# Kernel optimization log

Hardware: AMD Instinct MI355X
Metric: run time of the kernel (lower is better)

## Reference

```python
import jax, jax.numpy as jnp
import numpy as np

SCALING = 128.0 / 64  # alpha / rank = 2.0
EPS = 1e-8


def setup_inputs() -> dict:
    key = jax.random.key(0)
    ks = jax.random.split(key, 5)
    B, S, D_IN, D_OUT, R = 2, 4096, 4096, 4096, 64
    x = jax.random.normal(ks[0], (B, S, D_IN), dtype=jnp.float32)
    base_output = jax.random.normal(ks[1], (B, S, D_OUT), dtype=jnp.float32)
    base_weight = jax.random.normal(ks[2], (D_OUT, D_IN), dtype=jnp.float32) * 0.02
    lora_A = jax.random.normal(ks[3], (R, D_IN), dtype=jnp.float32) * 0.02
    lora_B = jax.random.normal(ks[4], (D_OUT, R), dtype=jnp.float32) * 0.02
    magnitude = jnp.ones((D_OUT,), dtype=jnp.float32)
    return {"x": x, "base_output": base_output, "base_weight": base_weight,
            "lora_A": lora_A, "lora_B": lora_B, "magnitude": magnitude}


def reference(x, base_output, base_weight, lora_A, lora_B, magnitude):
    # LoRA path: x @ A^T @ B^T, scaled  (dropout p=0 -> identity)
    xa = jnp.einsum('bsd,rd->bsr', x, lora_A)          # [B,S,r]
    delta_v = jnp.einsum('bsr,or->bso', xa, lora_B) * SCALING  # [B,S,out]
    # Updated weight and its per-row L2 norm
    updated_weight = base_weight + (lora_B @ lora_A) * SCALING  # [out,in]
    updated_norm = jnp.sqrt(jnp.sum(updated_weight * updated_weight, axis=1))  # [out]
    mag_scale = magnitude / (updated_norm + EPS)  # [out]
    combined = base_output + delta_v
    return combined * mag_scale[None, None, :]
```

## Files before the change

### kernel.cpp

```cpp
#include <hip/hip_runtime.h>
#include <math.h>

typedef __bf16 bf16x8 __attribute__((ext_vector_type(8)));
typedef float f32x4 __attribute__((ext_vector_type(4)));

#define MFMA16(a, b, c) __builtin_amdgcn_mfma_f32_16x16x32_bf16(a, b, c, 0, 0, 0)

static constexpr int M_TOT = 8192;
static constexpr int DIN = 4096;
static constexpr int DOUT = 4096;
static constexpr int RNK = 64;

__device__ inline unsigned short f2bf(float f) {
    union { float f; unsigned u; } v; v.f = f;
    unsigned r = v.u + 0x7FFFu + ((v.u >> 16) & 1u);
    return (unsigned short)(r >> 16);
}

__global__ __launch_bounds__(256) void k_prep(const float* __restrict__ A,
                                              const float* __restrict__ B,
                                              unsigned short* __restrict__ Afrag,
                                              unsigned short* __restrict__ Atfrag,
                                              unsigned short* __restrict__ Bfrag) {
    int i = blockIdx.x * 256 + threadIdx.x;
    unsigned short ab = f2bf(A[i]);
    int n = i >> 12, k = i & 4095;
    Afrag[(((k >> 5) << 2) + (n >> 4)) * 512 +
          ((((k >> 3) & 3) << 4) + (n & 15)) * 8 + (k & 7)] = ab;
    Atfrag[(((k >> 4) << 1) + (n >> 5)) * 512 +
           ((((n >> 3) & 3) << 4) + (k & 15)) * 8 + (n & 7)] = ab;
    unsigned short bb = f2bf(B[i]);
    int o = i >> 6, r = i & 63;
    Bfrag[(((o >> 4) << 1) + (r >> 5)) * 512 +
          ((((r >> 3) & 3) << 4) + (o & 15)) * 8 + (r & 7)] = bb;
}

__global__ __launch_bounds__(512, 6) void kA(const float* __restrict__ x,
                                             const unsigned short* __restrict__ Afrag,
                                             unsigned short* __restrict__ xafrag,
                                             const float* __restrict__ bw,
                                             const unsigned short* __restrict__ Bfrag,
                                             const unsigned short* __restrict__ Atfrag,
                                             const float* __restrict__ mag,
                                             float* __restrict__ mscale) {
    __shared__ __align__(16) char smem[33792];
    int tid = threadIdx.x;
    int wid = tid >> 6, lane = tid & 63;
    int row = lane & 15, kq = lane >> 4;
    int sr = tid >> 5, sc = (tid & 31) * 4;
    int lane8 = lane * 8;

    if (blockIdx.x < 512) {
        unsigned short (*stage)[520] = (unsigned short (*)[520])smem;
        float (*red)[1024] = (float (*)[1024])smem;
        int m0 = blockIdx.x * 16;
        const float* xrow = x + (size_t)(m0 + sr) * DIN + sc;

        f32x4 acc0 = {0.f, 0.f, 0.f, 0.f};
        f32x4 acc1 = acc0, acc2 = acc0, acc3 = acc0;

        f32x4 r0 = *(const f32x4*)(xrow);
        f32x4 r1 = *(const f32x4*)(xrow + 128);
        f32x4 r2 = *(const f32x4*)(xrow + 256);
        f32x4 r3 = *(const f32x4*)(xrow + 384);

        for (int c = 0; c < 8; ++c) {
            __syncthreads();
            ushort4 h;
            h.x = f2bf(r0[0]); h.y = f2bf(r0[1]); h.z = f2bf(r0[2]); h.w = f2bf(r0[3]);
            *(ushort4*)&stage[sr][sc] = h;
            h.x = f2bf(r1[0]); h.y = f2bf(r1[1]); h.z = f2bf(r1[2]); h.w = f2bf(r1[3]);
            *(ushort4*)&stage[sr][128 + sc] = h;
            h.x = f2bf(r2[0]); h.y = f2bf(r2[1]); h.z = f2bf(r2[2]); h.w = f2bf(r2[3]);
            *(ushort4*)&stage[sr][256 + sc] = h;
            h.x = f2bf(r3[0]); h.y = f2bf(r3[1]); h.z = f2bf(r3[2]); h.w = f2bf(r3[3]);
            *(ushort4*)&stage[sr][384 + sc] = h;
            if (c < 7) {
                const float* nx = xrow + (c + 1) * 512;
                r0 = *(const f32x4*)(nx);
                r1 = *(const f32x4*)(nx + 128);
                r2 = *(const f32x4*)(nx + 256);
                r3 = *(const f32x4*)(nx + 384);
            }
            __syncthreads();
            #pragma unroll
            for (int s = 0; s < 2; ++s) {
                int k0 = wid * 64 + s * 32;
                bf16x8 af = *(const bf16x8*)&stage[row][k0 + kq * 8];
                int ks = (c * 512 + k0) >> 5;
                const unsigned short* ap = Afrag + (size_t)(ks << 2) * 512 + lane8;
                acc0 = MFMA16(af, *(const bf16x8*)(ap), acc0);
                acc1 = MFMA16(af, *(const bf16x8*)(ap + 512), acc1);
                acc2 = MFMA16(af, *(const bf16x8*)(ap + 1024), acc2);
                acc3 = MFMA16(af, *(const bf16x8*)(ap + 1536), acc3);
            }
        }
        __syncthreads();

        int mb = kq * 4;
        #pragma unroll
        for (int rg = 0; rg < 4; ++rg) {
            red[wid][(mb + rg) * 64 + row]      = acc0[rg];
            red[wid][(mb + rg) * 64 + 16 + row] = acc1[rg];
            red[wid][(mb + rg) * 64 + 32 + row] = acc2[rg];
            red[wid][(mb + rg) * 64 + 48 + row] = acc3[rg];
        }
        __syncthreads();
        #pragma unroll
        for (int e = tid; e < 1024; e += 512) {
            float s = 0.f;
            #pragma unroll
            for (int w = 0; w < 8; ++w) s += red[w][e];
            int ml = e >> 6, r = e & 63;
            xafrag[((size_t)blockIdx.x * 2 + (r >> 5)) * 512 +
                   ((((r >> 3) & 3) << 4) + ml) * 8 + (r & 7)] = f2bf(s);
        }
    } else {
        float (*stagef)[516] = (float (*)[516])smem;
        float (*part)[16] = (float (*)[16])(smem + 33024);
        int o0 = (blockIdx.x - 512) * 16;
        int ot = o0 >> 4;

        bf16x8 b0 = *(const bf16x8*)(Bfrag + (size_t)(ot * 2) * 512 + lane8);
        bf16x8 b1 = *(const bf16x8*)(Bfrag + (size_t)(ot * 2 + 1) * 512 + lane8);

        f32x4 nacc = {0.f, 0.f, 0.f, 0.f};
        const float* bwrow = bw + (size_t)(o0 + sr) * DIN + sc;

        f32x4 q0 = *(const f32x4*)(bwrow);
        f32x4 q1 = *(const f32x4*)(bwrow + 128);
        f32x4 q2 = *(const f32x4*)(bwrow + 256);
        f32x4 q3 = *(const f32x4*)(bwrow + 384);

        for (int c = 0; c < 8; ++c) {
            __syncthreads();
            *(f32x4*)&stagef[sr][sc]       = q0;
            *(f32x4*)&stagef[sr][128 + sc] = q1;
            *(f32x4*)&stagef[sr][256 + sc] = q2;
            *(f32x4*)&stagef[sr][384 + sc] = q3;
            if (c < 7) {
                const float* nb = bwrow + (c + 1) * 512;
                q0 = *(const f32x4*)(nb);
                q1 = *(const f32x4*)(nb + 128);
                q2 = *(const f32x4*)(nb + 256);
                q3 = *(const f32x4*)(nb + 384);
            }
            __syncthreads();
            #pragma unroll
            for (int g = 0; g < 4; ++g) {
                int iloc = wid * 64 + g * 16;
                int it = (c * 512 + iloc) >> 4;
                const unsigned short* atp = Atfrag + (size_t)(it * 2) * 512 + lane8;
                bf16x8 a0 = *(const bf16x8*)(atp);
                bf16x8 a1 = *(const bf16x8*)(atp + 512);
                f32x4 d = {0.f, 0.f, 0.f, 0.f};
                d = MFMA16(a0, b0, d);
                d = MFMA16(a1, b1, d);
                f32x4 wv = *(const f32x4*)&stagef[row][iloc + kq * 4];
                #pragma unroll
                for (int rg = 0; rg < 4; ++rg) {
                    float w = wv[rg] + 2.0f * d[rg];
                    nacc[rg] += w * w;
                }
            }
        }
        float ns = nacc[0] + nacc[1] + nacc[2] + nacc[3];
        ns += __shfl_xor(ns, 16, 64);
        ns += __shfl_xor(ns, 32, 64);
        if (kq == 0) part[wid][row] = ns;
        __syncthreads();
        if (tid < 16) {
            float n2 = 0.f;
            #pragma unroll
            for (int w = 0; w < 8; ++w) n2 += part[w][tid];
            mscale[o0 + tid] = mag[o0 + tid] / (sqrtf(n2) + 1e-8f);
        }
    }
}

__global__ __launch_bounds__(256) void kB(const float* __restrict__ base,
                                          const unsigned short* __restrict__ xafrag,
                                          const unsigned short* __restrict__ Bfrag,
                                          const float* __restrict__ mscale,
                                          float* __restrict__ out) {
    __shared__ float dls[32][260];
    int tid = threadIdx.x;
    int wid = tid >> 6, lane = tid & 63;
    int row = lane & 15, kq = lane >> 4;
    int m0 = blockIdx.x * 32;
    int n0 = blockIdx.y * 256;
    int col = n0 + lane * 4;
    int lane8 = lane * 8;

    f32x4 bpre[2][4];
    #pragma unroll
    for (int h = 0; h < 2; ++h)
        #pragma unroll
        for (int r = 0; r < 4; ++r)
            bpre[h][r] = __builtin_nontemporal_load(
                (const f32x4*)(base + (size_t)(m0 + h * 16 + wid * 4 + r) * DOUT + col));
    f32x4 msv = *(const f32x4*)(mscale + col);

    bf16x8 xb0[2], xb1[2];
    #pragma unroll
    for (int h = 0; h < 2; ++h) {
        size_t mt = (size_t)(blockIdx.x * 2 + h);
        xb0[h] = *(const bf16x8*)(xafrag + (mt * 2) * 512 + lane8);
        xb1[h] = *(const bf16x8*)(xafrag + (mt * 2 + 1) * 512 + lane8);
    }

    #pragma unroll
    for (int nt = 0; nt < 4; ++nt) {
        size_t ntg = (size_t)((n0 + wid * 64 + nt * 16) >> 4);
        bf16x8 a0 = *(const bf16x8*)(Bfrag + (ntg * 2) * 512 + lane8);
        bf16x8 a1 = *(const bf16x8*)(Bfrag + (ntg * 2 + 1) * 512 + lane8);
        #pragma unroll
        for (int h = 0; h < 2; ++h) {
            f32x4 acc = {0.f, 0.f, 0.f, 0.f};
            acc = MFMA16(a0, xb0[h], acc);
            acc = MFMA16(a1, xb1[h], acc);
            *(f32x4*)&dls[h * 16 + row][wid * 64 + nt * 16 + kq * 4] = acc;
        }
    }
    __syncthreads();

    #pragma unroll
    for (int h = 0; h < 2; ++h)
        #pragma unroll
        for (int r = 0; r < 4; ++r) {
            int m = h * 16 + wid * 4 + r;
            f32x4 d = *(const f32x4*)&dls[m][lane * 4];
            size_t gidx = (size_t)(m0 + m) * DOUT + col;
            f32x4 o;
            #pragma unroll
            for (int j = 0; j < 4; ++j) o[j] = (bpre[h][r][j] + 2.0f * d[j]) * msv[j];
            __builtin_nontemporal_store(o, (f32x4*)(out + gidx));
        }
}

extern "C" void kernel_launch(void* const* d_in, const int* in_sizes, int n_in,
                              void* d_out, int out_size, void* d_ws, size_t ws_size,
                              hipStream_t stream) {
    const float* x    = (const float*)d_in[0];
    const float* base = (const float*)d_in[1];
    const float* bw   = (const float*)d_in[2];
    const float* lA   = (const float*)d_in[3];
    const float* lB   = (const float*)d_in[4];
    const float* mag  = (const float*)d_in[5];
    float* out = (float*)d_out;

    char* ws = (char*)d_ws;
    unsigned short* Afrag  = (unsigned short*)(ws);
    unsigned short* Atfrag = (unsigned short*)(ws + (512u << 10));
    unsigned short* Bfrag  = (unsigned short*)(ws + (1024u << 10));
    unsigned short* xafrag = (unsigned short*)(ws + (1536u << 10));
    float*          msc    = (float*)(ws + (2560u << 10));

    hipLaunchKernelGGL(k_prep, dim3(1024), dim3(256), 0, stream, lA, lB, Afrag, Atfrag, Bfrag);
    hipLaunchKernelGGL(kA, dim3(512 + 256), dim3(512), 0, stream,
                       x, Afrag, xafrag, bw, Bfrag, Atfrag, mag, msc);
    hipLaunchKernelGGL(kB, dim3(M_TOT / 32, DOUT / 256), dim3(256), 0, stream,
                       base, xafrag, Bfrag, msc, out);
}
```

Measured before the change: 112.1 us.

## Split-K the xA and weight-norm passes into separate wider kernels

Replaces the fused kA kernel with two split-K kernels. k1_xa splits the 4096-wide reduction over x into 4 parts, writes fp32 partials, and a small k1_fin kernel sums them into the bf16 fragment layout. k2_norm splits the weight-norm row reduction into 8 parts, and kB now sums those partials and computes the magnitude scale inline. The aim is more blocks with one-shot loads instead of a serial 8-chunk loop, giving more parallelism and latency hiding. The cost is an extra launch, an 8 MB round trip of fp32 partials, and redundant norm finalisation in every kB block.

```diff
diff --git a/kernel.cpp b/kernel.cpp
--- a/kernel.cpp
+++ b/kernel.cpp
@@ -35,153 +35,143 @@
           ((((r >> 3) & 3) << 4) + (o & 15)) * 8 + (r & 7)] = bb;
 }
 
-__global__ __launch_bounds__(512, 6) void kA(const float* __restrict__ x,
-                                             const unsigned short* __restrict__ Afrag,
-                                             unsigned short* __restrict__ xafrag,
-                                             const float* __restrict__ bw,
-                                             const unsigned short* __restrict__ Bfrag,
-                                             const unsigned short* __restrict__ Atfrag,
-                                             const float* __restrict__ mag,
-                                             float* __restrict__ mscale) {
-    __shared__ __align__(16) char smem[33792];
+__global__ __launch_bounds__(256, 4) void k1_xa(const float* __restrict__ x,
+                                                const unsigned short* __restrict__ Afrag,
+                                                float* __restrict__ pxa) {
+    __shared__ __align__(16) char smem[33024];
+    unsigned short (*stage)[1032] = (unsigned short (*)[1032])smem;
+    float (*red)[1024] = (float (*)[1024])smem;
     int tid = threadIdx.x;
     int wid = tid >> 6, lane = tid & 63;
     int row = lane & 15, kq = lane >> 4;
-    int sr = tid >> 5, sc = (tid & 31) * 4;
     int lane8 = lane * 8;
-
-    if (blockIdx.x < 512) {
-        unsigned short (*stage)[520] = (unsigned short (*)[520])smem;
-        float (*red)[1024] = (float (*)[1024])smem;
-        int m0 = blockIdx.x * 16;
-        const float* xrow = x + (size_t)(m0 + sr) * DIN + sc;
-
-        f32x4 acc0 = {0.f, 0.f, 0.f, 0.f};
-        f32x4 acc1 = acc0, acc2 = acc0, acc3 = acc0;
-
-        f32x4 r0 = *(const f32x4*)(xrow);
-        f32x4 r1 = *(const f32x4*)(xrow + 128);
-        f32x4 r2 = *(const f32x4*)(xrow + 256);
-        f32x4 r3 = *(const f32x4*)(xrow + 384);
-
-        for (int c = 0; c < 8; ++c) {
-            __syncthreads();
-            ushort4 h;
-            h.x = f2bf(r0[0]); h.y = f2bf(r0[1]); h.z = f2bf(r0[2]); h.w = f2bf(r0[3]);
-            *(ushort4*)&stage[sr][sc] = h;
-            h.x = f2bf(r1[0]); h.y = f2bf(r1[1]); h.z = f2bf(r1[2]); h.w = f2bf(r1[3]);
-            *(ushort4*)&stage[sr][128 + sc] = h;
-            h.x = f2bf(r2[0]); h.y = f2bf(r2[1]); h.z = f2bf(r2[2]); h.w = f2bf(r2[3]);
-            *(ushort4*)&stage[sr][256 + sc] = h;
-            h.x = f2bf(r3[0]); h.y = f2bf(r3[1]); h.z = f2bf(r3[2]); h.w = f2bf(r3[3]);
-            *(ushort4*)&stage[sr][384 + sc] = h;
-            if (c < 7) {
-                const float* nx = xrow + (c + 1) * 512;
-                r0 = *(const f32x4*)(nx);
-                r1 = *(const f32x4*)(nx + 128);
-                r2 = *(const f32x4*)(nx + 256);
-                r3 = *(const f32x4*)(nx + 384);
-            }
-            __syncthreads();
-            #pragma unroll
-            for (int s = 0; s < 2; ++s) {
-                int k0 = wid * 64 + s * 32;
-                bf16x8 af = *(const bf16x8*)&stage[row][k0 + kq * 8];
-                int ks = (c * 512 + k0) >> 5;
-                const unsigned short* ap = Afrag + (size_t)(ks << 2) * 512 + lane8;
-                acc0 = MFMA16(af, *(const bf16x8*)(ap), acc0);
-                acc1 = MFMA16(af, *(const bf16x8*)(ap + 512), acc1);
-                acc2 = MFMA16(af, *(const bf16x8*)(ap + 1024), acc2);
-                acc3 = MFMA16(af, *(const bf16x8*)(ap + 1536), acc3);
-            }
+    int mt = blockIdx.x & 511, kpart = blockIdx.x >> 9;
+    int m0 = mt * 16;
+    int sr = tid >> 4, sc = (tid & 15) * 4;
+
+    const float* xp = x + (size_t)(m0 + sr) * DIN + kpart * 1024 + sc;
+    f32x4 r[16];
+    #pragma unroll
+    for (int p = 0; p < 16; ++p) r[p] = *(const f32x4*)(xp + p * 64);
+
+    #pragma unroll
+    for (int p = 0; p < 16; ++p) {
+        ushort4 h;
+        h.x = f2bf(r[p][0]); h.y = f2bf(r[p][1]); h.z = f2bf(r[p][2]); h.w = f2bf(r[p][3]);
+        *(ushort4*)&stage[sr][p * 64 + sc] = h;
+    }
+    __syncthreads();
+
+    f32x4 acc0 = {0.f, 0.f, 0.f, 0.f};
+    f32x4 acc1 = acc0, acc2 = acc0, acc3 = acc0;
+    #pragma unroll
+    for (int s = 0; s < 8; ++s) {
+        bf16x8 af = *(const bf16x8*)&stage[row][wid * 256 + s * 32 + kq * 8];
+        int ks = kpart * 32 + wid * 8 + s;
+        const unsigned short* ap = Afrag + (size_t)(ks << 2) * 512 + lane8;
+        acc0 = MFMA16(af, *(const bf16x8*)(ap), acc0);
+        acc1 = MFMA16(af, *(const bf16x8*)(ap + 512), acc1);
+        acc2 = MFMA16(af, *(const bf16x8*)(ap + 1024), acc2);
+        acc3 = MFMA16(af, *(const bf16x8*)(ap + 1536), acc3);
+    }
+    __syncthreads();
+
+    int mb = kq * 4;
+    #pragma unroll
+    for (int rg = 0; rg < 4; ++rg) {
+        red[wid][(mb + rg) * 64 + row]      = acc0[rg];
+        red[wid][(mb + rg) * 64 + 16 + row] = acc1[rg];
+        red[wid][(mb + rg) * 64 + 32 + row] = acc2[rg];
+        red[wid][(mb + rg) * 64 + 48 + row] = acc3[rg];
+    }
+    __syncthreads();
+    #pragma unroll
+    for (int e = tid; e < 1024; e += 256) {
+        float s = red[0][e] + red[1][e] + red[2][e] + red[3][e];
+        pxa[(size_t)kpart * M_TOT * RNK + (size_t)(m0 + (e >> 6)) * RNK + (e & 63)] = s;
+    }
+}
+
+__global__ __launch_bounds__(256) void k1_fin(const float* __restrict__ pxa,
+                                              unsigned short* __restrict__ xafrag) {
+    int tid = threadIdx.x;
+    int mt = blockIdx.x;
+    int e0 = tid * 4;
+    size_t o = (size_t)(mt * 16 + (e0 >> 6)) * RNK + (e0 & 63);
+    f32x4 s0 = *(const f32x4*)(pxa + o);
+    f32x4 s1 = *(const f32x4*)(pxa + (size_t)M_TOT * RNK + o);
+    f32x4 s2 = *(const f32x4*)(pxa + 2 * (size_t)M_TOT * RNK + o);
+    f32x4 s3 = *(const f32x4*)(pxa + 3 * (size_t)M_TOT * RNK + o);
+    int ml = e0 >> 6, r0 = e0 & 63;
+    ushort4 h;
+    h.x = f2bf(s0[0] + s1[0] + s2[0] + s3[0]);
+    h.y = f2bf(s0[1] + s1[1] + s2[1] + s3[1]);
+    h.z = f2bf(s0[2] + s1[2] + s2[2] + s3[2]);
+    h.w = f2bf(s0[3] + s1[3] + s2[3] + s3[3]);
+    *(ushort4*)&xafrag[((size_t)(mt * 2 + (r0 >> 5))) * 512 +
+                       ((((r0 >> 3) & 3) << 4) + ml) * 8 + (r0 & 7)] = h;
+}
+
+__global__ __launch_bounds__(256, 4) void k2_norm(const float* __restrict__ bw,
+                                                  const unsigned short* __restrict__ Bfrag,
+                                                  const unsigned short* __restrict__ Atfrag,
+                                                  float* __restrict__ pn) {
+    __shared__ __align__(16) char smem[33280];
+    float (*stagef)[516] = (float (*)[516])smem;
+    float (*part)[16] = (float (*)[16])(smem + 33024);
+    int tid = threadIdx.x;
+    int wid = tid >> 6, lane = tid & 63;
+    int row = lane & 15, kq = lane >> 4;
+    int lane8 = lane * 8;
+    int ot = blockIdx.x & 255, ipart = blockIdx.x >> 8;
+    int o0 = ot * 16;
+    int sr = tid >> 4, sc = (tid & 15) * 4;
+
+    const float* bwp = bw + (size_t)(o0 + sr) * DIN + ipart * 512 + sc;
+    f32x4 q[8];
+    #pragma unroll
+    for (int p = 0; p < 8; ++p) q[p] = *(const f32x4*)(bwp + p * 64);
+
+    bf16x8 b0 = *(const bf16x8*)(Bfrag + (size_t)(ot * 2) * 512 + lane8);
+    bf16x8 b1 = *(const bf16x8*)(Bfrag + (size_t)(ot * 2 + 1) * 512 + lane8);
+
+    #pragma unroll
+    for (int p = 0; p < 8; ++p) *(f32x4*)&stagef[sr][p * 64 + sc] = q[p];
+    __syncthreads();
+
+    f32x4 nacc = {0.f, 0.f, 0.f, 0.f};
+    #pragma unroll
+    for (int g = 0; g < 8; ++g) {
+        int iloc = wid * 128 + g * 16;
+        int it = (ipart * 512 + iloc) >> 4;
+        const unsigned short* atp = Atfrag + (size_t)(it * 2) * 512 + lane8;
+        bf16x8 a0 = *(const bf16x8*)(atp);
+        bf16x8 a1 = *(const bf16x8*)(atp + 512);
+        f32x4 d = {0.f, 0.f, 0.f, 0.f};
+        d = MFMA16(a0, b0, d);
+        d = MFMA16(a1, b1, d);
+        f32x4 wv = *(const f32x4*)&stagef[row][iloc + kq * 4];
+        #pragma unroll
+        for (int rg = 0; rg < 4; ++rg) {
+            float w = wv[rg] + 2.0f * d[rg];
+            nacc[rg] += w * w;
         }
-        __syncthreads();
-
-        int mb = kq * 4;
-        #pragma unroll
-        for (int rg = 0; rg < 4; ++rg) {
-            red[wid][(mb + rg) * 64 + row]      = acc0[rg];
-            red[wid][(mb + rg) * 64 + 16 + row] = acc1[rg];
-            red[wid][(mb + rg) * 64 + 32 + row] = acc2[rg];
-            red[wid][(mb + rg) * 64 + 48 + row] = acc3[rg];
-        }
-        __syncthreads();
-        #pragma unroll
-        for (int e = tid; e < 1024; e += 512) {
-            float s = 0.f;
-            #pragma unroll
-            for (int w = 0; w < 8; ++w) s += red[w][e];
-            int ml = e >> 6, r = e & 63;
-            xafrag[((size_t)blockIdx.x * 2 + (r >> 5)) * 512 +
-                   ((((r >> 3) & 3) << 4) + ml) * 8 + (r & 7)] = f2bf(s);
-        }
-    } else {
-        float (*stagef)[516] = (float (*)[516])smem;
-        float (*part)[16] = (float (*)[16])(smem + 33024);
-        int o0 = (blockIdx.x - 512) * 16;
-        int ot = o0 >> 4;
-
-        bf16x8 b0 = *(const bf16x8*)(Bfrag + (size_t)(ot * 2) * 512 + lane8);
-        bf16x8 b1 = *(const bf16x8*)(Bfrag + (size_t)(ot * 2 + 1) * 512 + lane8);
-
-        f32x4 nacc = {0.f, 0.f, 0.f, 0.f};
-        const float* bwrow = bw + (size_t)(o0 + sr) * DIN + sc;
-
-        f32x4 q0 = *(const f32x4*)(bwrow);
-        f32x4 q1 = *(const f32x4*)(bwrow + 128);
-        f32x4 q2 = *(const f32x4*)(bwrow + 256);
-        f32x4 q3 = *(const f32x4*)(bwrow + 384);
-
-        for (int c = 0; c < 8; ++c) {
-            __syncthreads();
-            *(f32x4*)&stagef[sr][sc]       = q0;
-            *(f32x4*)&stagef[sr][128 + sc] = q1;
-            *(f32x4*)&stagef[sr][256 + sc] = q2;
-            *(f32x4*)&stagef[sr][384 + sc] = q3;
-            if (c < 7) {
-                const float* nb = bwrow + (c + 1) * 512;
-                q0 = *(const f32x4*)(nb);
-                q1 = *(const f32x4*)(nb + 128);
-                q2 = *(const f32x4*)(nb + 256);
-                q3 = *(const f32x4*)(nb + 384);
-            }
-            __syncthreads();
-            #pragma unroll
-            for (int g = 0; g < 4; ++g) {
-                int iloc = wid * 64 + g * 16;
-                int it = (c * 512 + iloc) >> 4;
-                const unsigned short* atp = Atfrag + (size_t)(it * 2) * 512 + lane8;
-                bf16x8 a0 = *(const bf16x8*)(atp);
-                bf16x8 a1 = *(const bf16x8*)(atp + 512);
-                f32x4 d = {0.f, 0.f, 0.f, 0.f};
-                d = MFMA16(a0, b0, d);
-                d = MFMA16(a1, b1, d);
-                f32x4 wv = *(const f32x4*)&stagef[row][iloc + kq * 4];
-                #pragma unroll
-                for (int rg = 0; rg < 4; ++rg) {
-                    float w = wv[rg] + 2.0f * d[rg];
-                    nacc[rg] += w * w;
-                }
-            }
-        }
-        float ns = nacc[0] + nacc[1] + nacc[2] + nacc[3];
-        ns += __shfl_xor(ns, 16, 64);
-        ns += __shfl_xor(ns, 32, 64);
-        if (kq == 0) part[wid][row] = ns;
-        __syncthreads();
-        if (tid < 16) {
-            float n2 = 0.f;
-            #pragma unroll
-            for (int w = 0; w < 8; ++w) n2 += part[w][tid];
-            mscale[o0 + tid] = mag[o0 + tid] / (sqrtf(n2) + 1e-8f);
-        }
-    }
+    }
+    float ns = nacc[0] + nacc[1] + nacc[2] + nacc[3];
+    ns += __shfl_xor(ns, 16, 64);
+    ns += __shfl_xor(ns, 32, 64);
+    if (kq == 0) part[wid][row] = ns;
+    __syncthreads();
+    if (tid < 16)
+        pn[ipart * DOUT + o0 + tid] =
+            part[0][tid] + part[1][tid] + part[2][tid] + part[3][tid];
 }
 
 __global__ __launch_bounds__(256) void kB(const float* __restrict__ base,
                                           const unsigned short* __restrict__ xafrag,
                                           const unsigned short* __restrict__ Bfrag,
-                                          const float* __restrict__ mscale,
+                                          const float* __restrict__ pn,
+                                          const float* __restrict__ mag,
                                           float* __restrict__ out) {
     __shared__ float dls[32][260];
     int tid = threadIdx.x;
@@ -199,7 +189,10 @@
         for (int r = 0; r < 4; ++r)
             bpre[h][r] = __builtin_nontemporal_load(
                 (const f32x4*)(base + (size_t)(m0 + h * 16 + wid * 4 + r) * DOUT + col));
-    f32x4 msv = *(const f32x4*)(mscale + col);
+    f32x4 pnv[8];
+    #pragma unroll
+    for (int p = 0; p < 8; ++p) pnv[p] = *(const f32x4*)(pn + p * DOUT + col);
+    f32x4 mg = *(const f32x4*)(mag + col);
 
     bf16x8 xb0[2], xb1[2];
     #pragma unroll
@@ -223,6 +216,15 @@
         }
     }
     __syncthreads();
+
+    f32x4 msv;
+    #pragma unroll
+    for (int j = 0; j < 4; ++j) {
+        float n2 = 0.f;
+        #pragma unroll
+        for (int p = 0; p < 8; ++p) n2 += pnv[p][j];
+        msv[j] = mg[j] / (sqrtf(n2) + 1e-8f);
+    }
 
     #pragma unroll
     for (int h = 0; h < 2; ++h)
@@ -254,11 +256,13 @@
     unsigned short* Atfrag = (unsigned short*)(ws + (512u << 10));
     unsigned short* Bfrag  = (unsigned short*)(ws + (1024u << 10));
     unsigned short* xafrag = (unsigned short*)(ws + (1536u << 10));
-    float*          msc    = (float*)(ws + (2560u << 10));
+    float*          pxa    = (float*)(ws + (2560u << 10));
+    float*          pn     = (float*)(ws + (10752u << 10));
 
     hipLaunchKernelGGL(k_prep, dim3(1024), dim3(256), 0, stream, lA, lB, Afrag, Atfrag, Bfrag);
-    hipLaunchKernelGGL(kA, dim3(512 + 256), dim3(512), 0, stream,
-                       x, Afrag, xafrag, bw, Bfrag, Atfrag, mag, msc);
+    hipLaunchKernelGGL(k1_xa, dim3(2048), dim3(256), 0, stream, x, Afrag, pxa);
+    hipLaunchKernelGGL(k2_norm, dim3(2048), dim3(256), 0, stream, bw, Bfrag, Atfrag, pn);
+    hipLaunchKernelGGL(k1_fin, dim3(512), dim3(256), 0, stream, pxa, xafrag);
     hipLaunchKernelGGL(kB, dim3(M_TOT / 32, DOUT / 256), dim3(256), 0, stream,
-                       base, xafrag, Bfrag, msc, out);
-}
+                       base, xafrag, Bfrag, pn, mag, out);
+}
```

Measured after the change: 134.8 us. +20.2%, slower.
